# Performance work log

Measured on AMD Instinct MI355X. Metric: run time of the kernel, lower is better.

The kernel has to match this reference:

```python
import jax, jax.numpy as jnp
import numpy as np

TAU = 2.0          # LIF membrane time constant (tau=2.0 in module)
SG_ALPHA = 4.0     # spikingjelly default Sigmoid surrogate alpha


def lif(x, v_th=1.0):
    """MultiStepLIFNode: leaky-integrate-fire over leading time dim T.
    v <- v + (x - v)/tau ; spike = H(v - v_th) ; hard reset v <- 0 where spiked.
    Surrogate gradient (sigmoid) via straight-through for backward.
    x: [T, ...] -> spikes: [T, ...]
    """
    def step(v, xt):
        v = v + (xt - v) / TAU
        sg = jax.nn.sigmoid(SG_ALPHA * (v - v_th))
        hard = (v >= v_th).astype(xt.dtype)
        spike = jax.lax.stop_gradient(hard - sg) + sg
        # detach_reset=True: reset path does not carry gradient
        v = v * (1.0 - jax.lax.stop_gradient(spike))
        return v, spike
    v0 = jnp.zeros_like(x[0])
    _, s = jax.lax.scan(step, v0, x)
    return s


def bn_c(x, scale, bias):
    """Inference-mode BatchNorm folded to per-channel affine; x: [T,B,C,N]."""
    return x * scale[None, None, :, None] + bias[None, None, :, None]


def setup_inputs() -> dict:
    T, B, C, H, W = 4, 32, 512, 14, 14
    Ch = int(C * 4.0)  # mlp hidden
    key = jax.random.key(0)
    ks = jax.random.split(key, 16)
    std = 0.05
    d = {
        'x': jax.random.normal(ks[0], (T, B, C, H, W), jnp.float32),
        'q_w': jax.random.normal(ks[1], (C, C), jnp.float32) * std,
        'q_bn_s': 1.0 + 0.1 * jax.random.normal(ks[2], (C,), jnp.float32),
        'q_bn_b': 0.1 * jax.random.normal(ks[3], (C,), jnp.float32),
        'k_w': jax.random.normal(ks[4], (C, C), jnp.float32) * std,
        'k_bn_s': 1.0 + 0.1 * jax.random.normal(ks[5], (C,), jnp.float32),
        'k_bn_b': 0.1 * jax.random.normal(ks[6], (C,), jnp.float32),
        'proj_w': jax.random.normal(ks[7], (C, C), jnp.float32) * std,
        'proj_b': 0.1 * jax.random.normal(ks[8], (C,), jnp.float32),
        'proj_bn_s': 1.0 + 0.1 * jax.random.normal(ks[9], (C,), jnp.float32),
        'proj_bn_b': 0.1 * jax.random.normal(ks[10], (C,), jnp.float32),
        'mlp1_w': jax.random.normal(ks[11], (Ch, C), jnp.float32) * std,
        'mlp1_b': 0.1 * jax.random.normal(ks[12], (Ch,), jnp.float32),
        'mlp1_bn_s': 1.0 + 0.1 * jax.random.normal(ks[13], (Ch,), jnp.float32),
        'mlp1_bn_b': 0.1 * jax.random.normal(ks[14], (Ch,), jnp.float32),
        'mlp2_w': jax.random.normal(ks[15], (C, Ch), jnp.float32) * std,
        'mlp2_b': 0.1 * jax.random.normal(jax.random.fold_in(key, 100), (C,), jnp.float32),
        'mlp2_bn_s': 1.0 + 0.1 * jax.random.normal(jax.random.fold_in(key, 101), (C,), jnp.float32),
        'mlp2_bn_b': 0.1 * jax.random.normal(jax.random.fold_in(key, 102), (C,), jnp.float32),
    }
    return d


NUM_HEADS = 8


def reference(x, q_w, q_bn_s, q_bn_b, k_w, k_bn_s, k_bn_b,
              proj_w, proj_b, proj_bn_s, proj_bn_b,
              mlp1_w, mlp1_b, mlp1_bn_s, mlp1_bn_b,
              mlp2_w, mlp2_b, mlp2_bn_s, mlp2_bn_b):
    T, B, C, H, W = x.shape
    N = H * W
    h = NUM_HEADS
    Chd = C // h
    xf = x.reshape(T, B, C, N)

    # ---- Token_QK_Attention ----
    q_sp = lif(bn_c(jnp.einsum('oc,tbcn->tbon', q_w, xf), q_bn_s, q_bn_b))
    k_sp = lif(bn_c(jnp.einsum('oc,tbcn->tbon', k_w, xf), k_bn_s, k_bn_b))
    # per-head channel sum of q spikes: [T,B,h,1,N]
    q_sum = q_sp.reshape(T, B, h, Chd, N).sum(axis=3, keepdims=True)
    attn_sp = lif(q_sum, v_th=0.5)                       # attn_lif, v_threshold=0.5
    x_one = attn_sp * k_sp.reshape(T, B, h, Chd, N)      # spiking multiply
    x_one = x_one.reshape(T, B, C, N)
    p = jnp.einsum('oc,tbcn->tbon', proj_w, x_one) + proj_b[None, None, :, None]
    y = lif(bn_c(p, proj_bn_s, proj_bn_b)).reshape(T, B, C, H, W)
    x = x + y                                            # residual

    # ---- MLP ----
    xf = x.reshape(T, B, C, N)
    h1 = jnp.einsum('oc,tbcn->tbon', mlp1_w, xf) + mlp1_b[None, None, :, None]
    h1 = lif(bn_c(h1, mlp1_bn_s, mlp1_bn_b))
    h2 = jnp.einsum('oc,tbcn->tbon', mlp2_w, h1) + mlp2_b[None, None, :, None]
    h2 = lif(bn_c(h2, mlp2_bn_s, mlp2_bn_b))
    return x + h2.reshape(T, B, C, H, W)
```

## Files before the change

kernel.cpp:

```cpp
#include <hip/hip_runtime.h>
#include <cstdint>

#define NT  4
#define NB  32
#define NC  512
#define NCH 2048
#define NN  196
#define NM  (NB * NN)
#define NMB (NM / 8)
#define NH  8

struct GP {
    const float *q_bn_s, *q_bn_b, *k_bn_s, *k_bn_b;
    const float *proj_b, *proj_bn_s, *proj_bn_b;
    const float *mlp1_b, *mlp1_bn_s, *mlp1_bn_b;
    const float *mlp2_b, *mlp2_bn_s, *mlp2_bn_b;
    const float *wqkT, *wprojT, *wmlp1T, *wmlp2T;
    const float *xT;
    float *xy;
    float *v_q, *v_k, *v_y, *v_h1, *v_h2, *v_attn;
    unsigned char *q_bt, *k_bt, *h1_bt, *attn_bt;
    float *out;
    int t;
};

__device__ __forceinline__ float lif_step(float z, float v_old, float vth, int& sp) {
    float d = __fsub_rn(z, v_old);
    float h = __fmul_rn(d, 0.5f);
    float v = __fadd_rn(v_old, h);
    sp = (v >= vth) ? 1 : 0;
    return sp ? 0.0f : v;
}

typedef const void __attribute__((address_space(1))) gas_t;
typedef void __attribute__((address_space(3))) las_t;
__device__ __forceinline__ void gl_lds16(const float* g, float* l) {
    __builtin_amdgcn_global_load_lds((gas_t*)g, (las_t*)l, 16, 0, 0);
}
template <int N>
__device__ __forceinline__ void vmwait() {
    if constexpr (N == 0)      asm volatile("s_waitcnt vmcnt(0)" ::: "memory");
    else if constexpr (N == 3) asm volatile("s_waitcnt vmcnt(3)" ::: "memory");
    else if constexpr (N == 4) asm volatile("s_waitcnt vmcnt(4)" ::: "memory");
}
__device__ __forceinline__ void vm0() {
    asm volatile("s_waitcnt vmcnt(0)" ::: "memory");
}
__device__ __forceinline__ void lgkm0() {
    asm volatile("s_waitcnt lgkmcnt(0)" ::: "memory");
}


__global__ __launch_bounds__(256) void trw_k(const float* __restrict__ src,
                                             float* __restrict__ dst,
                                             int K, int ldD, int offD) {
    __shared__ float tle[32][33];
    const int c0 = blockIdx.x * 32, o0 = blockIdx.y * 32;
    const int tx = threadIdx.x & 31, ty = threadIdx.x >> 5;
#pragma unroll
    for (int r = 0; r < 4; ++r)
        tle[ty + r * 8][tx] = src[(size_t)(o0 + ty + r * 8) * K + c0 + tx];
    __syncthreads();
#pragma unroll
    for (int r = 0; r < 4; ++r)
        dst[(size_t)(c0 + ty + r * 8) * ldD + offD + o0 + tx] = tle[tx][ty + r * 8];
}

__global__ __launch_bounds__(64) void permx_k(const float* __restrict__ x,
                                              float* __restrict__ xT) {
    const int id = blockIdx.x;
    const int b = id & 31;
    const int c = (id >> 5) & 511;
    const int t = id >> 14;
    const float* s = x + ((size_t)(t * NB + b) * NC + c) * NN;
    float* d = xT + ((size_t)(t * NC + c) * NB + b) * NN;
    for (int n = threadIdx.x; n < NN; n += 64) d[n] = s[n];
}

__global__ __launch_bounds__(256) void attn_k(GP gp) {
    const int id = blockIdx.x * 256 + threadIdx.x;
    if (id >= NH * NMB) return;
    const int mB = id % NMB;
    const int h = id / NMB;
    int s[8];
#pragma unroll
    for (int j = 0; j < 8; ++j) s[j] = 0;
    const unsigned char* q = gp.q_bt + (size_t)(h * 64) * NMB + mB;
#pragma unroll 8
    for (int d = 0; d < 64; ++d) {
        const unsigned b = q[(size_t)d * NMB];
#pragma unroll
        for (int j = 0; j < 8; ++j) s[j] += (b >> j) & 1;
    }
    unsigned ob = 0;
#pragma unroll
    for (int j = 0; j < 8; ++j) {
        const int m = mB * 8 + j;
        float v = gp.t ? gp.v_attn[(size_t)h * NM + m] : 0.0f;
        int sp;
        v = lif_step((float)s[j], v, 0.5f, sp);
        gp.v_attn[(size_t)h * NM + m] = v;
        ob |= (unsigned)sp << j;
    }
    gp.attn_bt[(size_t)h * NMB + mB] = (unsigned char)ob;
}

template <int MODE>
__global__ __launch_bounds__(64) void gemm_unf(GP gp) {
    constexpr int LDA = (MODE == 0) ? 1024 : 2048;
    constexpr int BK = 16;
    constexpr int NIT = 512 / BK;

    __shared__ float As[2][BK][32];
    __shared__ float Xs[2][BK][64];

    const int lane = threadIdx.x;
    const int to = lane & 7;
    const int tn = lane >> 3;
    const int m0 = blockIdx.x * 64;
    const int ot = blockIdx.y;
    const int o0 = ot * 32;
    const int mb = m0 + tn * 8;
    const int mbB = (m0 >> 3) + tn;

    const float* wA = (MODE == 0) ? gp.wqkT : gp.wmlp1T;
    const float* xf = (MODE == 0) ? gp.xT + (size_t)gp.t * NC * NM : gp.xy;

    auto stageA = [&](int buf, int s) {
#pragma unroll
        for (int r = 0; r < 2; ++r)
            gl_lds16(wA + (size_t)(s * BK + r * 8 + (lane >> 3)) * LDA + o0 + (lane & 7) * 4,
                     &As[buf][r * 8][0]);
    };
    auto stageX = [&](int buf, int s) {
#pragma unroll
        for (int r = 0; r < 4; ++r)
            gl_lds16(xf + (size_t)(s * BK + r * 4 + (lane >> 4)) * NM + m0 + (lane & 15) * 4,
                     &Xs[buf][r * 4][0]);
    };

    float acc[4][8];
#pragma unroll
    for (int i = 0; i < 4; ++i)
#pragma unroll
        for (int j = 0; j < 8; ++j) acc[i][j] = 0.0f;

    auto compute = [&](int cur) {
#pragma unroll 4
        for (int kk = 0; kk < BK; ++kk) {
            const float4 av = *(const float4*)&As[cur][kk][to * 4];
            const float4 x0 = *(const float4*)&Xs[cur][kk][tn * 8];
            const float4 x1 = *(const float4*)&Xs[cur][kk][tn * 8 + 4];
            const float a4[4] = {av.x, av.y, av.z, av.w};
            const float x8[8] = {x0.x, x0.y, x0.z, x0.w, x1.x, x1.y, x1.z, x1.w};
#pragma unroll
            for (int i = 0; i < 4; ++i)
#pragma unroll
                for (int j = 0; j < 8; ++j)
                    acc[i][j] = __fadd_rn(acc[i][j], __fmul_rn(a4[i], x8[j]));
        }
    };

    stageA(0, 0); stageX(0, 0);
    vm0();
#pragma unroll 1
    for (int it = 0; it < NIT; ++it) {
        const int cur = it & 1;
        const bool more = (it + 1 < NIT);
        if (more) { stageA(cur ^ 1, it + 1); stageX(cur ^ 1, it + 1); }
        compute(cur);
        if (more) vm0();
    }

    if constexpr (MODE == 0) {
        const bool isq = (ot < 16);
        const float* bs = isq ? gp.q_bn_s : gp.k_bn_s;
        const float* bbv = isq ? gp.q_bn_b : gp.k_bn_b;
        float* vb = isq ? gp.v_q : gp.v_k;
        unsigned char* sb = isq ? gp.q_bt : gp.k_bt;
        const int ob = (ot & 15) * 32;
#pragma unroll
        for (int i = 0; i < 4; ++i) {
            const int oo = ob + to * 4 + i;
            const float sc = bs[oo], bc = bbv[oo];
            float* vr = vb + (size_t)oo * NM + mb;
            float vv[8];
            if (gp.t) {
                const float4 v0 = *(const float4*)vr, v1 = *(const float4*)(vr + 4);
                vv[0] = v0.x; vv[1] = v0.y; vv[2] = v0.z; vv[3] = v0.w;
                vv[4] = v1.x; vv[5] = v1.y; vv[6] = v1.z; vv[7] = v1.w;
            } else {
#pragma unroll
                for (int j = 0; j < 8; ++j) vv[j] = 0.0f;
            }
            unsigned pb = 0;
#pragma unroll
            for (int j = 0; j < 8; ++j) {
                const float z = __fadd_rn(__fmul_rn(acc[i][j], sc), bc);
                int sp;
                vv[j] = lif_step(z, vv[j], 1.0f, sp);
                pb |= (unsigned)sp << j;
            }
            *(float4*)vr = make_float4(vv[0], vv[1], vv[2], vv[3]);
            *(float4*)(vr + 4) = make_float4(vv[4], vv[5], vv[6], vv[7]);
            sb[(size_t)oo * NMB + mbB] = (unsigned char)pb;
        }
    } else {
        const int ob = ot * 32;
#pragma unroll
        for (int i = 0; i < 4; ++i) {
            const int o = ob + to * 4 + i;
            const float bi = gp.mlp1_b[o], sc = gp.mlp1_bn_s[o], bc = gp.mlp1_bn_b[o];
            float* vr = gp.v_h1 + (size_t)o * NM + mb;
            float vv[8];
            if (gp.t) {
                const float4 v0 = *(const float4*)vr, v1 = *(const float4*)(vr + 4);
                vv[0] = v0.x; vv[1] = v0.y; vv[2] = v0.z; vv[3] = v0.w;
                vv[4] = v1.x; vv[5] = v1.y; vv[6] = v1.z; vv[7] = v1.w;
            } else {
#pragma unroll
                for (int j = 0; j < 8; ++j) vv[j] = 0.0f;
            }
            unsigned pb = 0;
#pragma unroll
            for (int j = 0; j < 8; ++j) {
                const float z = __fadd_rn(__fmul_rn(__fadd_rn(acc[i][j], bi), sc), bc);
                int sp;
                vv[j] = lif_step(z, vv[j], 1.0f, sp);
                pb |= (unsigned)sp << j;
            }
            *(float4*)vr = make_float4(vv[0], vv[1], vv[2], vv[3]);
            *(float4*)(vr + 4) = make_float4(vv[4], vv[5], vv[6], vv[7]);
            gp.h1_bt[(size_t)o * NMB + mbB] = (unsigned char)pb;
        }
    }
}

template <int MODE>
__global__ __launch_bounds__(64) void gemm_fus(GP gp) {
    constexpr int K_TOT = (MODE == 3) ? 2048 : 512;
    constexpr int BK = 16;
    constexpr int NIT = K_TOT / BK;
    constexpr int STW = (MODE == 1) ? 4 : 3;

    __shared__ float As[4][BK][32];
    __shared__ float Xs[4][BK][36];

    const int lane = threadIdx.x;
    const int to = lane & 7;
    const int tn = lane >> 3;
    const int m0 = blockIdx.x * 32;
    const int o0 = blockIdx.y * 32;
    const int mb = m0 + tn * 4;

    const float* wA = (MODE == 1) ? gp.wprojT : gp.wmlp2T;

    const int xrow = lane >> 2;
    const int xby = lane & 3;
    const int mB8 = (m0 >> 3) + xby;

    auto stageA = [&](int buf, int s) {
#pragma unroll
        for (int r = 0; r < 2; ++r)
            gl_lds16(wA + (size_t)(s * BK + r * 8 + (lane >> 3)) * 512 + o0 + (lane & 7) * 4,
                     &As[buf][r * 8][0]);
    };
    auto loadB = [&](int s) -> uint2 {
        const int c = s * BK + xrow;
        uint2 r;
        if constexpr (MODE == 1) {
            r.x = gp.k_bt[(size_t)c * NMB + mB8];
            r.y = gp.attn_bt[(size_t)(c >> 6) * NMB + mB8];
        } else {
            r.x = gp.h1_bt[(size_t)c * NMB + mB8];
            r.y = 0;
        }
        return r;
    };
    auto flushB = [&](int buf, uint2 xb) {
        const unsigned w = (MODE == 1) ? (xb.x & xb.y) : xb.x;
        float* d = &Xs[buf][xrow][xby * 8];
        float4 f0, f1;
        f0.x = (float)((w) & 1);
        f0.y = (float)((w >> 1) & 1);
        f0.z = (float)((w >> 2) & 1);
        f0.w = (float)((w >> 3) & 1);
        f1.x = (float)((w >> 4) & 1);
        f1.y = (float)((w >> 5) & 1);
        f1.z = (float)((w >> 6) & 1);
        f1.w = (float)((w >> 7) & 1);
        *(float4*)d = f0;
        *(float4*)(d + 4) = f1;
    };

    float acc[4][4];
#pragma unroll
    for (int i = 0; i < 4; ++i)
#pragma unroll
        for (int j = 0; j < 4; ++j) acc[i][j] = 0.0f;

    auto compute = [&](int cb) {
#pragma unroll 8
        for (int kk = 0; kk < BK; ++kk) {
            const float4 av = *(const float4*)&As[cb][kk][to * 4];
            const float4 xv = *(const float4*)&Xs[cb][kk][tn * 4];
            const float a4[4] = {av.x, av.y, av.z, av.w};
            const float x4[4] = {xv.x, xv.y, xv.z, xv.w};
#pragma unroll
            for (int i = 0; i < 4; ++i)
#pragma unroll
                for (int j = 0; j < 4; ++j)
                    acc[i][j] = __fmaf_rn(a4[i], x4[j], acc[i][j]);
        }
    };

    uint2 sl0, sl1;
    stageA(0, 0); sl0 = loadB(0);
    stageA(1, 1); sl1 = loadB(1);
    vmwait<STW>();
    flushB(0, sl0);
    lgkm0();

    auto body = [&](int i, int cb, uint2& sStage, uint2& sFlush) {
        if (i + 2 < NIT) { stageA((cb + 2) & 3, i + 2); sStage = loadB(i + 2); }
        compute(cb);
        if (i + 1 < NIT) {
            if (NIT - 1 - i >= 2) vmwait<STW>(); else vmwait<0>();
            flushB((cb + 1) & 3, sFlush);
            lgkm0();
        }
    };
#pragma unroll 1
    for (int i = 0; i < NIT; i += 4) {
        body(i + 0, 0, sl0, sl1);
        body(i + 1, 1, sl1, sl0);
        body(i + 2, 2, sl0, sl1);
        body(i + 3, 3, sl1, sl0);
    }

    if constexpr (MODE == 1) {
#pragma unroll
        for (int i = 0; i < 4; ++i) {
            const int o = o0 + to * 4 + i;
            const float bi = gp.proj_b[o], sc = gp.proj_bn_s[o], bc = gp.proj_bn_b[o];
            float* vr = gp.v_y + (size_t)o * NM + mb;
            const float4 vld = gp.t ? *(const float4*)vr : make_float4(0, 0, 0, 0);
            const float4 xv4 = *(const float4*)(gp.xT + ((size_t)gp.t * NC + o) * NM + mb);
            float vv[4] = {vld.x, vld.y, vld.z, vld.w};
            const float xvv[4] = {xv4.x, xv4.y, xv4.z, xv4.w};
            float xyo[4];
#pragma unroll
            for (int j = 0; j < 4; ++j) {
                const float z = __fadd_rn(__fmul_rn(__fadd_rn(acc[i][j], bi), sc), bc);
                int sp;
                vv[j] = lif_step(z, vv[j], 1.0f, sp);
                xyo[j] = __fadd_rn(xvv[j], (float)sp);
            }
            *(float4*)vr = make_float4(vv[0], vv[1], vv[2], vv[3]);
            *(float4*)(gp.xy + (size_t)o * NM + mb) = make_float4(xyo[0], xyo[1], xyo[2], xyo[3]);
        }
    } else {
        const int b = mb / NN;
        const int n = mb - b * NN;
#pragma unroll
        for (int i = 0; i < 4; ++i) {
            const int o = o0 + to * 4 + i;
            const float bi = gp.mlp2_b[o], sc = gp.mlp2_bn_s[o], bc = gp.mlp2_bn_b[o];
            float* vr = gp.v_h2 + (size_t)o * NM + mb;
            const float4 vld = gp.t ? *(const float4*)vr : make_float4(0, 0, 0, 0);
            const float4 xyv = *(const float4*)(gp.xy + (size_t)o * NM + mb);
            float vv[4] = {vld.x, vld.y, vld.z, vld.w};
            const float xyf[4] = {xyv.x, xyv.y, xyv.z, xyv.w};
            float ov[4];
#pragma unroll
            for (int j = 0; j < 4; ++j) {
                const float z = __fadd_rn(__fmul_rn(__fadd_rn(acc[i][j], bi), sc), bc);
                int sp;
                vv[j] = lif_step(z, vv[j], 1.0f, sp);
                ov[j] = __fadd_rn(xyf[j], (float)sp);
            }
            *(float4*)&gp.out[(((size_t)gp.t * NB + b) * NC + o) * NN + n] =
                make_float4(ov[0], ov[1], ov[2], ov[3]);
            *(float4*)vr = make_float4(vv[0], vv[1], vv[2], vv[3]);
        }
    }
}

extern "C" void kernel_launch(void* const* d_in, const int* in_sizes, int n_in,
                              void* d_out, int out_size, void* d_ws, size_t ws_size,
                              hipStream_t stream) {
    const float* x       = (const float*)d_in[0];
    const float* q_w     = (const float*)d_in[1];
    const float* k_w     = (const float*)d_in[4];
    const float* proj_w  = (const float*)d_in[7];
    const float* mlp1_w  = (const float*)d_in[11];
    const float* mlp2_w  = (const float*)d_in[15];

    GP gp;
    gp.q_bn_s = (const float*)d_in[2];  gp.q_bn_b = (const float*)d_in[3];
    gp.k_bn_s = (const float*)d_in[5];  gp.k_bn_b = (const float*)d_in[6];
    gp.proj_b = (const float*)d_in[8];  gp.proj_bn_s = (const float*)d_in[9];  gp.proj_bn_b = (const float*)d_in[10];
    gp.mlp1_b = (const float*)d_in[12]; gp.mlp1_bn_s = (const float*)d_in[13]; gp.mlp1_bn_b = (const float*)d_in[14];
    gp.mlp2_b = (const float*)d_in[16]; gp.mlp2_bn_s = (const float*)d_in[17]; gp.mlp2_bn_b = (const float*)d_in[18];
    gp.out = (float*)d_out;

    char* ws = (char*)d_ws;
    size_t off = 0;
    auto alloc = [&](size_t bytes) -> void* {
        void* r = ws + off;
        off += (bytes + 255) & ~(size_t)255;
        return r;
    };
    float* wqkT   = (float*)alloc((size_t)512 * 1024 * 4);
    float* wprojT = (float*)alloc((size_t)512 * 512 * 4);
    float* wmlp1T = (float*)alloc((size_t)512 * 2048 * 4);
    float* wmlp2T = (float*)alloc((size_t)2048 * 512 * 4);
    float* xT     = (float*)alloc((size_t)NT * NC * NM * 4);
    gp.xy     = (float*)alloc((size_t)NC * NM * 4);
    gp.v_q    = (float*)alloc((size_t)NC * NM * 4);
    gp.v_k    = (float*)alloc((size_t)NC * NM * 4);
    gp.v_y    = (float*)alloc((size_t)NC * NM * 4);
    gp.v_h2   = (float*)alloc((size_t)NC * NM * 4);
    gp.v_h1   = (float*)alloc((size_t)NCH * NM * 4);
    gp.v_attn = (float*)alloc((size_t)NH * NM * 4);
    gp.q_bt   = (unsigned char*)alloc((size_t)NC * NMB);
    gp.k_bt   = (unsigned char*)alloc((size_t)NC * NMB);
    gp.h1_bt  = (unsigned char*)alloc((size_t)NCH * NMB);
    gp.attn_bt= (unsigned char*)alloc((size_t)NH * NMB);
    gp.wqkT = wqkT; gp.wprojT = wprojT; gp.wmlp1T = wmlp1T; gp.wmlp2T = wmlp2T;
    gp.xT = xT;

    trw_k<<<dim3(16, 16), 256, 0, stream>>>(q_w,    wqkT,   512,  1024, 0);
    trw_k<<<dim3(16, 16), 256, 0, stream>>>(k_w,    wqkT,   512,  1024, 512);
    trw_k<<<dim3(16, 16), 256, 0, stream>>>(proj_w, wprojT, 512,  512,  0);
    trw_k<<<dim3(16, 64), 256, 0, stream>>>(mlp1_w, wmlp1T, 512,  2048, 0);
    trw_k<<<dim3(64, 16), 256, 0, stream>>>(mlp2_w, wmlp2T, 2048, 512,  0);
    permx_k<<<NT * NC * NB, 64, 0, stream>>>(x, xT);

    for (int t = 0; t < NT; ++t) {
        gp.t = t;
        gemm_unf<0><<<dim3(98, 32), 64, 0, stream>>>(gp);
        attn_k<<<dim3(25), 256, 0, stream>>>(gp);
        gemm_fus<1><<<dim3(196, 16), 64, 0, stream>>>(gp);
        gemm_unf<2><<<dim3(98, 64), 64, 0, stream>>>(gp);
        gemm_fus<3><<<dim3(196, 16), 64, 0, stream>>>(gp);
    }
}
```

Before: 2.557 ms.

## Transpose spike bitmaps to token-major and keep packed bits in LDS

Spike bitmaps for q, k, h1 and attn now use a token-major layout ([m-byte][channel]) instead of channel-major. The GEMM epilogues pack four output channels into one 32-bit store, attn_k sums head channels with SWAR popcount over word loads, and gemm_fus keeps the packed bytes in LDS, expanding bits to floats in registers. This targets scattered byte stores, strided loads, and the LDS footprint and write traffic of the float-expanded B tile. The costs are extra integer unpacking in the inner FMA loop and far fewer attn_k threads (4 blocks of 256 threads), which limits parallelism in that kernel.

```diff
diff --git a/kernel.cpp b/kernel.cpp
--- a/kernel.cpp
+++ b/kernel.cpp
@@ -78,31 +78,39 @@
 }
 
 __global__ __launch_bounds__(256) void attn_k(GP gp) {
-    const int id = blockIdx.x * 256 + threadIdx.x;
-    if (id >= NH * NMB) return;
-    const int mB = id % NMB;
-    const int h = id / NMB;
-    int s[8];
-#pragma unroll
-    for (int j = 0; j < 8; ++j) s[j] = 0;
-    const unsigned char* q = gp.q_bt + (size_t)(h * 64) * NMB + mB;
-#pragma unroll 8
-    for (int d = 0; d < 64; ++d) {
-        const unsigned b = q[(size_t)d * NMB];
-#pragma unroll
-        for (int j = 0; j < 8; ++j) s[j] += (b >> j) & 1;
-    }
-    unsigned ob = 0;
-#pragma unroll
-    for (int j = 0; j < 8; ++j) {
-        const int m = mB * 8 + j;
-        float v = gp.t ? gp.v_attn[(size_t)h * NM + m] : 0.0f;
-        int sp;
-        v = lif_step((float)s[j], v, 0.5f, sp);
-        gp.v_attn[(size_t)h * NM + m] = v;
-        ob |= (unsigned)sp << j;
-    }
-    gp.attn_bt[(size_t)h * NMB + mB] = (unsigned char)ob;
+    const int mB = blockIdx.x * 256 + threadIdx.x;
+    if (mB >= NMB) return;
+    const unsigned* qr = (const unsigned*)(gp.q_bt + (size_t)mB * NC);
+    unsigned outB[8];
+#pragma unroll
+    for (int h = 0; h < NH; ++h) {
+        unsigned a[8];
+#pragma unroll
+        for (int j = 0; j < 8; ++j) a[j] = 0;
+#pragma unroll
+        for (int d = 0; d < 16; ++d) {
+            const unsigned w = qr[h * 16 + d];
+#pragma unroll
+            for (int j = 0; j < 8; ++j) a[j] += (w >> j) & 0x01010101u;
+        }
+        float* vr = gp.v_attn + (size_t)h * NM + mB * 8;
+        unsigned ob = 0;
+#pragma unroll
+        for (int j = 0; j < 8; ++j) {
+            unsigned s = a[j] + (a[j] >> 16);
+            s = (s + (s >> 8)) & 0xff;
+            float v = gp.t ? vr[j] : 0.0f;
+            int sp;
+            v = lif_step((float)s, v, 0.5f, sp);
+            vr[j] = v;
+            ob |= (unsigned)sp << j;
+        }
+        outB[h] = ob;
+    }
+    uint2 w;
+    w.x = outB[0] | (outB[1] << 8) | (outB[2] << 16) | (outB[3] << 24);
+    w.y = outB[4] | (outB[5] << 8) | (outB[6] << 16) | (outB[7] << 24);
+    *(uint2*)(gp.attn_bt + (size_t)mB * 8) = w;
 }
 
 template <int MODE>
@@ -179,6 +187,7 @@
         float* vb = isq ? gp.v_q : gp.v_k;
         unsigned char* sb = isq ? gp.q_bt : gp.k_bt;
         const int ob = (ot & 15) * 32;
+        unsigned pw = 0;
 #pragma unroll
         for (int i = 0; i < 4; ++i) {
             const int oo = ob + to * 4 + i;
@@ -203,10 +212,12 @@
             }
             *(float4*)vr = make_float4(vv[0], vv[1], vv[2], vv[3]);
             *(float4*)(vr + 4) = make_float4(vv[4], vv[5], vv[6], vv[7]);
-            sb[(size_t)oo * NMB + mbB] = (unsigned char)pb;
-        }
+            pw |= pb << (i * 8);
+        }
+        *(unsigned*)(sb + (size_t)mbB * NC + ob + to * 4) = pw;
     } else {
         const int ob = ot * 32;
+        unsigned pw = 0;
 #pragma unroll
         for (int i = 0; i < 4; ++i) {
             const int o = ob + to * 4 + i;
@@ -231,8 +242,9 @@
             }
             *(float4*)vr = make_float4(vv[0], vv[1], vv[2], vv[3]);
             *(float4*)(vr + 4) = make_float4(vv[4], vv[5], vv[6], vv[7]);
-            gp.h1_bt[(size_t)o * NMB + mbB] = (unsigned char)pb;
-        }
+            pw |= pb << (i * 8);
+        }
+        *(unsigned*)(gp.h1_bt + (size_t)mbB * NCH + ob + to * 4) = pw;
     }
 }
 
@@ -244,7 +256,7 @@
     constexpr int STW = (MODE == 1) ? 4 : 3;
 
     __shared__ float As[4][BK][32];
-    __shared__ float Xs[4][BK][36];
+    __shared__ unsigned char Xb[4][4][16];
 
     const int lane = threadIdx.x;
     const int to = lane & 7;
@@ -252,12 +264,15 @@
     const int m0 = blockIdx.x * 32;
     const int o0 = blockIdx.y * 32;
     const int mb = m0 + tn * 4;
+    const int mB0 = m0 >> 3;
+    const unsigned nib = 4u * (tn & 1);
 
     const float* wA = (MODE == 1) ? gp.wprojT : gp.wmlp2T;
-
-    const int xrow = lane >> 2;
-    const int xby = lane & 3;
-    const int mB8 = (m0 >> 3) + xby;
+    const unsigned char* xbt = (MODE == 1) ? gp.k_bt : gp.h1_bt;
+
+    const int l4 = lane & 15;
+    const int mbi = l4 >> 2;
+    const int rr = l4 & 3;
 
     auto stageA = [&](int buf, int s) {
 #pragma unroll
@@ -266,31 +281,17 @@
                      &As[buf][r * 8][0]);
     };
     auto loadB = [&](int s) -> uint2 {
-        const int c = s * BK + xrow;
         uint2 r;
-        if constexpr (MODE == 1) {
-            r.x = gp.k_bt[(size_t)c * NMB + mB8];
-            r.y = gp.attn_bt[(size_t)(c >> 6) * NMB + mB8];
-        } else {
-            r.x = gp.h1_bt[(size_t)c * NMB + mB8];
+        r.x = *(const unsigned*)(xbt + (size_t)(mB0 + mbi) * K_TOT + s * BK + rr * 4);
+        if constexpr (MODE == 1)
+            r.y = gp.attn_bt[(size_t)(mB0 + mbi) * 8 + (s >> 2)];
+        else
             r.y = 0;
-        }
         return r;
     };
     auto flushB = [&](int buf, uint2 xb) {
-        const unsigned w = (MODE == 1) ? (xb.x & xb.y) : xb.x;
-        float* d = &Xs[buf][xrow][xby * 8];
-        float4 f0, f1;
-        f0.x = (float)((w) & 1);
-        f0.y = (float)((w >> 1) & 1);
-        f0.z = (float)((w >> 2) & 1);
-        f0.w = (float)((w >> 3) & 1);
-        f1.x = (float)((w >> 4) & 1);
-        f1.y = (float)((w >> 5) & 1);
-        f1.z = (float)((w >> 6) & 1);
-        f1.w = (float)((w >> 7) & 1);
-        *(float4*)d = f0;
-        *(float4*)(d + 4) = f1;
+        const unsigned w = (MODE == 1) ? (xb.x & (xb.y * 0x01010101u)) : xb.x;
+        *(unsigned*)&Xb[buf][mbi][rr * 4] = w;
     };
 
     float acc[4][4];
@@ -300,12 +301,16 @@
         for (int j = 0; j < 4; ++j) acc[i][j] = 0.0f;
 
     auto compute = [&](int cb) {
-#pragma unroll 8
+        const uint4 xq = *(const uint4*)&Xb[cb][tn >> 1][0];
+        const unsigned xs[4] = {xq.x >> nib, xq.y >> nib, xq.z >> nib, xq.w >> nib};
+#pragma unroll
         for (int kk = 0; kk < BK; ++kk) {
             const float4 av = *(const float4*)&As[cb][kk][to * 4];
-            const float4 xv = *(const float4*)&Xs[cb][kk][tn * 4];
             const float a4[4] = {av.x, av.y, av.z, av.w};
-            const float x4[4] = {xv.x, xv.y, xv.z, xv.w};
+            const unsigned wsel = xs[kk >> 2] >> ((kk & 3) * 8);
+            float x4[4];
+#pragma unroll
+            for (int j = 0; j < 4; ++j) x4[j] = (float)((wsel >> j) & 1u);
 #pragma unroll
             for (int i = 0; i < 4; ++i)
 #pragma unroll
@@ -423,10 +428,10 @@
     gp.v_h2   = (float*)alloc((size_t)NC * NM * 4);
     gp.v_h1   = (float*)alloc((size_t)NCH * NM * 4);
     gp.v_attn = (float*)alloc((size_t)NH * NM * 4);
-    gp.q_bt   = (unsigned char*)alloc((size_t)NC * NMB);
-    gp.k_bt   = (unsigned char*)alloc((size_t)NC * NMB);
-    gp.h1_bt  = (unsigned char*)alloc((size_t)NCH * NMB);
-    gp.attn_bt= (unsigned char*)alloc((size_t)NH * NMB);
+    gp.q_bt   = (unsigned char*)alloc((size_t)NMB * NC);
+    gp.k_bt   = (unsigned char*)alloc((size_t)NMB * NC);
+    gp.h1_bt  = (unsigned char*)alloc((size_t)NMB * NCH);
+    gp.attn_bt= (unsigned char*)alloc((size_t)NMB * NH);
     gp.wqkT = wqkT; gp.wprojT = wprojT; gp.wmlp1T = wmlp1T; gp.wmlp2T = wmlp2T;
     gp.xT = xT;
 
@@ -440,7 +445,7 @@
     for (int t = 0; t < NT; ++t) {
         gp.t = t;
         gemm_unf<0><<<dim3(98, 32), 64, 0, stream>>>(gp);
-        attn_k<<<dim3(25), 256, 0, stream>>>(gp);
+        attn_k<<<dim3(4), 256, 0, stream>>>(gp);
         gemm_fus<1><<<dim3(196, 16), 64, 0, stream>>>(gp);
         gemm_unf<2><<<dim3(98, 64), 64, 0, stream>>>(gp);
         gemm_fus<3><<<dim3(196, 16), 64, 0, stream>>>(gp);
```

Result: slower. 3.696 ms (+44.5%).
